# Kernel tuning notes

Hardware: AMD Instinct MI355X
Metric: run time of the kernel (lower is better)

## Reference

```python
import jax, jax.numpy as jnp
import numpy as np

UNITS = 1024


def setup_inputs() -> dict:
    key = jax.random.key(0)
    k1, k2, k3, k4, k5 = jax.random.split(key, 5)
    scale = 1.0 / np.sqrt(UNITS)
    return {
        "s_prev": jax.random.normal(k1, (32, UNITS), jnp.float32),
        "hidden_states": jax.random.normal(k2, (32, 4096, UNITS), jnp.float32),
        "W_w": jax.random.normal(k3, (UNITS, UNITS), jnp.float32) * scale,
        "W_b": jnp.zeros((UNITS,), jnp.float32),
        "U_w": jax.random.normal(k4, (UNITS, UNITS), jnp.float32) * scale,
        "U_b": jnp.zeros((UNITS,), jnp.float32),
        "V_w": jax.random.normal(k5, (UNITS, 1), jnp.float32) * scale,
        "V_b": jnp.zeros((1,), jnp.float32),
    }


def reference(s_prev, hidden_states, W_w, W_b, U_w, U_b, V_w, V_b):
    # s_prev: [B, U]; hidden_states: [B, S, U]
    w_s = s_prev @ W_w + W_b                      # [B, U]
    u_h = jnp.einsum("bsu,uv->bsv", hidden_states, U_w) + U_b  # [B, S, U]
    score = jnp.tanh(w_s[:, None, :] + u_h) @ V_w + V_b        # [B, S, 1]
    weights = jax.nn.softmax(score, axis=1)       # [B, S, 1]
    context = jnp.sum(weights * hidden_states, axis=1)         # [B, U]
    return context, weights
```

## Files before the change

kernel.cpp:

```cpp
#include <hip/hip_runtime.h>
#include <hip/hip_bf16.h>
#include <stdint.h>

typedef __attribute__((ext_vector_type(8))) short bf16x8;
typedef __attribute__((ext_vector_type(4))) float f32x4;
typedef __attribute__((ext_vector_type(2))) float f32x2;
typedef __attribute__((ext_vector_type(4))) short short4v;

#define UNITS 1024
#define BATCH 32
#define SEQ 4096
#define CHUNK 64
#define NCHUNK (SEQ / CHUNK)
#define PAD 8
#define LDK (UNITS + PAD)

static __device__ __forceinline__ float bf2f(unsigned short u) {
    union { unsigned int i; float f; } x; x.i = ((unsigned int)u) << 16; return x.f;
}
static __device__ __forceinline__ unsigned short f2bf(float f) {
    __hip_bfloat16 h = __float2bfloat16(f);
    return *reinterpret_cast<unsigned short*>(&h);
}
static __device__ __forceinline__ float fast_tanh(float x) {
    float e = __expf(2.0f * x);
    return 1.0f - 2.0f / (e + 1.0f);
}

__global__ void k_transpose_cast(const float* __restrict__ Uw,
                                 unsigned short* __restrict__ UwT) {
    __shared__ float tile[32][33];
    const int ti = blockIdx.x, tj = blockIdx.y;
    const int c = threadIdx.x;
    const int r0 = threadIdx.y;
#pragma unroll
    for (int rr = 0; rr < 4; ++rr) {
        int r = r0 + rr * 8;
        tile[r][c] = Uw[(size_t)(ti * 32 + r) * UNITS + tj * 32 + c];
    }
    __syncthreads();
#pragma unroll
    for (int rr = 0; rr < 4; ++rr) {
        int rv = r0 + rr * 8;
        UwT[(size_t)(tj * 32 + rv) * UNITS + ti * 32 + c] = f2bf(tile[c][rv]);
    }
}

__global__ void k_ws(const float* __restrict__ s_prev, const float* __restrict__ Ww,
                     const float* __restrict__ Wb, const float* __restrict__ Ub,
                     float* __restrict__ ws_vec) {
    const int b = blockIdx.y;
    const int v = blockIdx.x * 256 + threadIdx.x;
    const float* sp = s_prev + (size_t)b * UNITS;
    float acc = 0.f;
#pragma unroll 4
    for (int u = 0; u < UNITS; ++u)
        acc = fmaf(sp[u], Ww[(size_t)u * UNITS + v], acc);
    ws_vec[(size_t)b * UNITS + v] = acc + Wb[v] + Ub[v];
}

__launch_bounds__(512, 2)
__global__ void k_score_ctx(const float* __restrict__ hidden,
                            const unsigned short* __restrict__ UwT,
                            const float* __restrict__ ws_vec,
                            const float* __restrict__ Vw,
                            const float* __restrict__ Vb,
                            float* __restrict__ scores,
                            float* __restrict__ mstat,
                            float* __restrict__ lstat,
                            float* __restrict__ ctx_part) {
    __shared__ unsigned short h_lds[CHUNK * LDK];
    __shared__ float ws_lds[UNITS];
    __shared__ float v_lds[UNITS];
    __shared__ float scpart[8][CHUNK];
    __shared__ float sc_lds[CHUNK];
    __shared__ float esc[CHUNK];

    const int tid = threadIdx.x;
    const int bx  = blockIdx.x;
    const int b     = bx / NCHUNK;
    const int chunk = bx % NCHUNK;
    const int lane = tid & 63;
    const int w    = tid >> 6;
    const int l15  = lane & 15;
    const int l4   = lane >> 4;

    for (int i = tid; i < UNITS; i += 512) {
        ws_lds[i] = ws_vec[(size_t)b * UNITS + i];
        v_lds[i]  = Vw[i];
    }
    {
        const float* hbase = hidden + ((size_t)b * SEQ + (size_t)chunk * CHUNK) * UNITS;
        const int c4 = (tid & 255) * 4;
        const int rhalf = tid >> 8;
#pragma unroll 4
        for (int i = 0; i < 32; ++i) {
            int r = i * 2 + rhalf;
            f32x4 v = *reinterpret_cast<const f32x4*>(hbase + (size_t)r * UNITS + c4);
            short4v p;
            p.x = (short)f2bf(v.x); p.y = (short)f2bf(v.y);
            p.z = (short)f2bf(v.z); p.w = (short)f2bf(v.w);
            *reinterpret_cast<short4v*>(&h_lds[r * LDK + c4]) = p;
        }
    }
    __syncthreads();

    float spart[4][4];
#pragma unroll
    for (int fr = 0; fr < 4; ++fr)
#pragma unroll
        for (int j = 0; j < 4; ++j) spart[fr][j] = 0.f;

    for (int outer = 0; outer < 2; ++outer) {
        const int col0 = outer * 512 + w * 64;
        f32x4 acc[4][4];
#pragma unroll
        for (int fr = 0; fr < 4; ++fr)
#pragma unroll
            for (int fc = 0; fc < 4; ++fc) acc[fr][fc] = (f32x4)(0.f);

        for (int k0 = 0; k0 < UNITS; k0 += 32) {
            bf16x8 af[4], bf[4];
#pragma unroll
            for (int fr = 0; fr < 4; ++fr)
                af[fr] = *reinterpret_cast<const bf16x8*>(
                    &h_lds[(fr * 16 + l15) * LDK + k0 + l4 * 8]);
#pragma unroll
            for (int fc = 0; fc < 4; ++fc)
                bf[fc] = *reinterpret_cast<const bf16x8*>(
                    &UwT[(size_t)(col0 + fc * 16 + l15) * UNITS + k0 + l4 * 8]);
#pragma unroll
            for (int fr = 0; fr < 4; ++fr)
#pragma unroll
                for (int fc = 0; fc < 4; ++fc)
                    acc[fr][fc] = __builtin_amdgcn_mfma_f32_16x16x32_bf16(
                        af[fr], bf[fc], acc[fr][fc], 0, 0, 0);
        }
#pragma unroll
        for (int fc = 0; fc < 4; ++fc) {
            const int col = col0 + fc * 16 + l15;
            const float wsv = ws_lds[col];
            const float vv  = v_lds[col];
#pragma unroll
            for (int fr = 0; fr < 4; ++fr)
#pragma unroll
                for (int j = 0; j < 4; ++j) {
                    float t = fast_tanh(wsv + acc[fr][fc][j]);
                    spart[fr][j] = fmaf(t, vv, spart[fr][j]);
                }
        }
    }
#pragma unroll
    for (int fr = 0; fr < 4; ++fr)
#pragma unroll
        for (int j = 0; j < 4; ++j) {
            float v = spart[fr][j];
            v += __shfl_xor(v, 1);
            v += __shfl_xor(v, 2);
            v += __shfl_xor(v, 4);
            v += __shfl_xor(v, 8);
            spart[fr][j] = v;
        }
    if (l15 == 0) {
#pragma unroll
        for (int fr = 0; fr < 4; ++fr)
#pragma unroll
            for (int j = 0; j < 4; ++j)
                scpart[w][fr * 16 + l4 * 4 + j] = spart[fr][j];
    }
    __syncthreads();

    if (tid < CHUNK) {
        float sc = Vb[0];
#pragma unroll
        for (int ww = 0; ww < 8; ++ww) sc += scpart[ww][tid];
        scores[(size_t)b * SEQ + chunk * CHUNK + tid] = sc;
        sc_lds[tid] = sc;
    }
    __syncthreads();

    if (tid < 64) {
        float v = sc_lds[tid];
        float m = v;
#pragma unroll
        for (int mk = 1; mk < 64; mk <<= 1) m = fmaxf(m, __shfl_xor(m, mk));
        float e = __expf(v - m);
        esc[tid] = e;
        float l = e;
#pragma unroll
        for (int mk = 1; mk < 64; mk <<= 1) l += __shfl_xor(l, mk);
        if (tid == 0) {
            mstat[b * NCHUNK + chunk] = m;
            lstat[b * NCHUNK + chunk] = l;
        }
    }
    __syncthreads();

    {
        const int u0 = tid * 2;
        float a0 = 0.f, a1 = 0.f;
#pragma unroll 8
        for (int s = 0; s < CHUNK; ++s) {
            unsigned int p = *reinterpret_cast<const unsigned int*>(&h_lds[s * LDK + u0]);
            float e = esc[s];
            a0 = fmaf(e, bf2f((unsigned short)(p & 0xffffu)), a0);
            a1 = fmaf(e, bf2f((unsigned short)(p >> 16)), a1);
        }
        f32x2 o; o.x = a0; o.y = a1;
        *reinterpret_cast<f32x2*>(&ctx_part[((size_t)(b * NCHUNK + chunk)) * UNITS + u0]) = o;
    }
}

__global__ void k_weights(const float* __restrict__ scores, float* __restrict__ out_w) {
    const int b = blockIdx.x;
    const int tid = threadIdx.x;
    __shared__ float red[8];
    float sc[16];
#pragma unroll
    for (int i = 0; i < 16; ++i) sc[i] = scores[(size_t)b * SEQ + tid + i * 256];
    float m = sc[0];
#pragma unroll
    for (int i = 1; i < 16; ++i) m = fmaxf(m, sc[i]);
#pragma unroll
    for (int mk = 1; mk < 64; mk <<= 1) m = fmaxf(m, __shfl_xor(m, mk));
    if ((tid & 63) == 0) red[tid >> 6] = m;
    __syncthreads();
    m = fmaxf(fmaxf(red[0], red[1]), fmaxf(red[2], red[3]));
    __syncthreads();
    float l = 0.f;
#pragma unroll
    for (int i = 0; i < 16; ++i) { sc[i] = __expf(sc[i] - m); l += sc[i]; }
#pragma unroll
    for (int mk = 1; mk < 64; mk <<= 1) l += __shfl_xor(l, mk);
    if ((tid & 63) == 0) red[tid >> 6] = l;
    __syncthreads();
    l = red[0] + red[1] + red[2] + red[3];
    const float inv = 1.0f / l;
#pragma unroll
    for (int i = 0; i < 16; ++i)
        out_w[(size_t)b * SEQ + tid + i * 256] = sc[i] * inv;
}

__global__ void k_ctx_reduce(const float* __restrict__ mstat, const float* __restrict__ lstat,
                             const float* __restrict__ ctx_part, float* __restrict__ out_ctx) {
    const int b = blockIdx.x;
    const int tid = threadIdx.x;
    __shared__ float m_l[NCHUNK], l_l[NCHUNK], f_l[NCHUNK];
    if (tid < NCHUNK) { m_l[tid] = mstat[b * NCHUNK + tid]; l_l[tid] = lstat[b * NCHUNK + tid]; }
    __syncthreads();
    float M = -1e30f;
#pragma unroll 8
    for (int c = 0; c < NCHUNK; ++c) M = fmaxf(M, m_l[c]);
    __syncthreads();
    if (tid < NCHUNK) f_l[tid] = __expf(m_l[tid] - M);
    __syncthreads();
    float L = 0.f;
#pragma unroll 8
    for (int c = 0; c < NCHUNK; ++c) L += f_l[c] * l_l[c];
    const float inv = 1.0f / L;
    const int u = tid * 4;
    f32x4 acc = (f32x4)(0.f);
    for (int c = 0; c < NCHUNK; ++c) {
        float f = f_l[c];
        f32x4 v = *reinterpret_cast<const f32x4*>(
            &ctx_part[((size_t)(b * NCHUNK + c)) * UNITS + u]);
        acc.x = fmaf(f, v.x, acc.x);
        acc.y = fmaf(f, v.y, acc.y);
        acc.z = fmaf(f, v.z, acc.z);
        acc.w = fmaf(f, v.w, acc.w);
    }
    acc.x *= inv; acc.y *= inv; acc.z *= inv; acc.w *= inv;
    *reinterpret_cast<f32x4*>(&out_ctx[(size_t)b * UNITS + u]) = acc;
}

extern "C" void kernel_launch(void* const* d_in, const int* in_sizes, int n_in,
                              void* d_out, int out_size, void* d_ws, size_t ws_size,
                              hipStream_t stream) {
    const float* s_prev = (const float*)d_in[0];
    const float* hidden = (const float*)d_in[1];
    const float* Ww     = (const float*)d_in[2];
    const float* Wb     = (const float*)d_in[3];
    const float* Uw     = (const float*)d_in[4];
    const float* Ub     = (const float*)d_in[5];
    const float* Vw     = (const float*)d_in[6];
    const float* Vb     = (const float*)d_in[7];

    float* out_ctx = (float*)d_out;
    float* out_w   = (float*)d_out + BATCH * UNITS;

    char* wsb = (char*)d_ws;
    unsigned short* UwT = (unsigned short*)wsb;
    float* ws_vec = (float*)(wsb + (2u << 20));
    float* scores = (float*)(wsb + (2u << 20) + 131072);
    float* mstat  = (float*)(wsb + (2u << 20) + 131072 + 524288);
    float* lstat  = mstat + BATCH * NCHUNK;
    float* ctx_part = lstat + BATCH * NCHUNK;

    hipLaunchKernelGGL(k_transpose_cast, dim3(32, 32), dim3(32, 8), 0, stream, Uw, UwT);
    hipLaunchKernelGGL(k_ws, dim3(4, 32), dim3(256), 0, stream, s_prev, Ww, Wb, Ub, ws_vec);
    hipLaunchKernelGGL(k_score_ctx, dim3(BATCH * NCHUNK), dim3(512), 0, stream,
                       hidden, UwT, ws_vec, Vw, Vb, scores, mstat, lstat, ctx_part);
    hipLaunchKernelGGL(k_weights, dim3(BATCH), dim3(256), 0, stream, scores, out_w);
    hipLaunchKernelGGL(k_ctx_reduce, dim3(BATCH), dim3(256), 0, stream,
                       mstat, lstat, ctx_part, out_ctx);
}
```

Measured before the change: 1.305 ms.

## Persistent multi-chunk score kernel with pipelined hidden loads; split-K w_s GEMV

The score/context kernel now runs 256 persistent blocks, each handling 8 consecutive chunks. Hidden-state K-tiles are prefetched into registers two tiles ahead and converted into LDS while the MFMA work for the first column half runs, so global load latency overlaps compute. The w_s GEMV becomes a split-K kernel that keeps weight slices in registers and reuses them across the batch, followed by a reduction kernel. The trade-off is fewer blocks in flight (256 on a large GPU), more barriers per chunk, and higher register pressure from the prefetch buffers.

```diff
diff --git a/kernel.cpp b/kernel.cpp
--- a/kernel.cpp
+++ b/kernel.cpp
@@ -14,6 +14,9 @@
 #define NCHUNK (SEQ / CHUNK)
 #define PAD 8
 #define LDK (UNITS + PAD)
+#define BK 128
+#define NKT (UNITS / BK)
+#define TASKS 8
 
 static __device__ __forceinline__ float bf2f(unsigned short u) {
     union { unsigned int i; float f; } x; x.i = ((unsigned int)u) << 16; return x.f;
@@ -46,17 +49,41 @@
     }
 }
 
-__global__ void k_ws(const float* __restrict__ s_prev, const float* __restrict__ Ww,
-                     const float* __restrict__ Wb, const float* __restrict__ Ub,
-                     float* __restrict__ ws_vec) {
-    const int b = blockIdx.y;
-    const int v = blockIdx.x * 256 + threadIdx.x;
-    const float* sp = s_prev + (size_t)b * UNITS;
-    float acc = 0.f;
-#pragma unroll 4
-    for (int u = 0; u < UNITS; ++u)
-        acc = fmaf(sp[u], Ww[(size_t)u * UNITS + v], acc);
-    ws_vec[(size_t)b * UNITS + v] = acc + Wb[v] + Ub[v];
+__global__ void k_ws_part(const float* __restrict__ s_prev, const float* __restrict__ Ww,
+                          float* __restrict__ part) {
+    const int ks = blockIdx.x;
+    const int col0 = threadIdx.x * 4;
+    f32x4 wreg[32];
+#pragma unroll
+    for (int u = 0; u < 32; ++u)
+        wreg[u] = *reinterpret_cast<const f32x4*>(&Ww[(size_t)(ks * 32 + u) * UNITS + col0]);
+    for (int b = 0; b < BATCH; ++b) {
+        f32x4 acc = (f32x4)(0.f);
+#pragma unroll
+        for (int u = 0; u < 32; ++u) {
+            const float s = s_prev[(size_t)b * UNITS + ks * 32 + u];
+            acc.x = fmaf(s, wreg[u].x, acc.x);
+            acc.y = fmaf(s, wreg[u].y, acc.y);
+            acc.z = fmaf(s, wreg[u].z, acc.z);
+            acc.w = fmaf(s, wreg[u].w, acc.w);
+        }
+        *reinterpret_cast<f32x4*>(&part[((size_t)b * 32 + ks) * UNITS + col0]) = acc;
+    }
+}
+
+__global__ void k_ws_red(const float* __restrict__ part, const float* __restrict__ Wb,
+                         const float* __restrict__ Ub, float* __restrict__ ws_vec) {
+    const int b = blockIdx.x;
+    const int col0 = threadIdx.x * 4;
+    f32x4 acc = *reinterpret_cast<const f32x4*>(&Wb[col0]);
+    f32x4 ub  = *reinterpret_cast<const f32x4*>(&Ub[col0]);
+    acc.x += ub.x; acc.y += ub.y; acc.z += ub.z; acc.w += ub.w;
+#pragma unroll
+    for (int ks = 0; ks < 32; ++ks) {
+        f32x4 p = *reinterpret_cast<const f32x4*>(&part[((size_t)b * 32 + ks) * UNITS + col0]);
+        acc.x += p.x; acc.y += p.y; acc.z += p.z; acc.w += p.w;
+    }
+    *reinterpret_cast<f32x4*>(&ws_vec[(size_t)b * UNITS + col0]) = acc;
 }
 
 __launch_bounds__(512, 2)
@@ -73,141 +100,180 @@
     __shared__ float ws_lds[UNITS];
     __shared__ float v_lds[UNITS];
     __shared__ float scpart[8][CHUNK];
-    __shared__ float sc_lds[CHUNK];
     __shared__ float esc[CHUNK];
 
     const int tid = threadIdx.x;
-    const int bx  = blockIdx.x;
-    const int b     = bx / NCHUNK;
-    const int chunk = bx % NCHUNK;
+    const int blk = blockIdx.x;
+    const int b      = blk >> 3;
+    const int chunk0 = (blk & 7) * TASKS;
     const int lane = tid & 63;
     const int w    = tid >> 6;
     const int l15  = lane & 15;
     const int l4   = lane >> 4;
+    const int srow = tid >> 5;
+    const int sc0  = (tid & 31) * 4;
 
     for (int i = tid; i < UNITS; i += 512) {
         ws_lds[i] = ws_vec[(size_t)b * UNITS + i];
         v_lds[i]  = Vw[i];
     }
-    {
-        const float* hbase = hidden + ((size_t)b * SEQ + (size_t)chunk * CHUNK) * UNITS;
-        const int c4 = (tid & 255) * 4;
-        const int rhalf = tid >> 8;
-#pragma unroll 4
-        for (int i = 0; i < 32; ++i) {
-            int r = i * 2 + rhalf;
-            f32x4 v = *reinterpret_cast<const f32x4*>(hbase + (size_t)r * UNITS + c4);
-            short4v p;
-            p.x = (short)f2bf(v.x); p.y = (short)f2bf(v.y);
-            p.z = (short)f2bf(v.z); p.w = (short)f2bf(v.w);
-            *reinterpret_cast<short4v*>(&h_lds[r * LDK + c4]) = p;
-        }
-    }
-    __syncthreads();
-
-    float spart[4][4];
-#pragma unroll
-    for (int fr = 0; fr < 4; ++fr)
-#pragma unroll
-        for (int j = 0; j < 4; ++j) spart[fr][j] = 0.f;
-
-    for (int outer = 0; outer < 2; ++outer) {
-        const int col0 = outer * 512 + w * 64;
-        f32x4 acc[4][4];
-#pragma unroll
-        for (int fr = 0; fr < 4; ++fr)
-#pragma unroll
-            for (int fc = 0; fc < 4; ++fc) acc[fr][fc] = (f32x4)(0.f);
-
-        for (int k0 = 0; k0 < UNITS; k0 += 32) {
-            bf16x8 af[4], bf[4];
+    const float vb0 = Vb[0];
+
+    auto issue = [&](const float* hb, int kt, f32x4* P) {
+#pragma unroll
+        for (int j = 0; j < 4; ++j)
+            P[j] = *reinterpret_cast<const f32x4*>(
+                hb + (size_t)(srow + j * 16) * UNITS + kt * BK + sc0);
+    };
+    auto swrite = [&](int kt, f32x4* P) {
+#pragma unroll
+        for (int j = 0; j < 4; ++j) {
+            short4v s;
+            s.x = (short)f2bf(P[j].x); s.y = (short)f2bf(P[j].y);
+            s.z = (short)f2bf(P[j].z); s.w = (short)f2bf(P[j].w);
+            *reinterpret_cast<short4v*>(&h_lds[(srow + j * 16) * LDK + kt * BK + sc0]) = s;
+        }
+    };
+    auto gemm_tile = [&](int kt, f32x4 (&acc)[4][4], int colbase) {
+#pragma unroll
+        for (int ks = 0; ks < 4; ++ks) {
+            const int k0 = kt * BK + ks * 32;
+            bf16x8 af[4], bfr[4];
 #pragma unroll
             for (int fr = 0; fr < 4; ++fr)
                 af[fr] = *reinterpret_cast<const bf16x8*>(
                     &h_lds[(fr * 16 + l15) * LDK + k0 + l4 * 8]);
 #pragma unroll
             for (int fc = 0; fc < 4; ++fc)
-                bf[fc] = *reinterpret_cast<const bf16x8*>(
-                    &UwT[(size_t)(col0 + fc * 16 + l15) * UNITS + k0 + l4 * 8]);
+                bfr[fc] = *reinterpret_cast<const bf16x8*>(
+                    &UwT[(size_t)(colbase + fc * 16 + l15) * UNITS + k0 + l4 * 8]);
 #pragma unroll
             for (int fr = 0; fr < 4; ++fr)
 #pragma unroll
                 for (int fc = 0; fc < 4; ++fc)
                     acc[fr][fc] = __builtin_amdgcn_mfma_f32_16x16x32_bf16(
-                        af[fr], bf[fc], acc[fr][fc], 0, 0, 0);
-        }
+                        af[fr], bfr[fc], acc[fr][fc], 0, 0, 0);
+        }
+    };
+    auto epi = [&](f32x4 (&acc)[4][4], int colbase, float (&spart)[4][4]) {
 #pragma unroll
         for (int fc = 0; fc < 4; ++fc) {
-            const int col = col0 + fc * 16 + l15;
+            const int col = colbase + fc * 16 + l15;
             const float wsv = ws_lds[col];
             const float vv  = v_lds[col];
 #pragma unroll
             for (int fr = 0; fr < 4; ++fr)
 #pragma unroll
-                for (int j = 0; j < 4; ++j) {
-                    float t = fast_tanh(wsv + acc[fr][fc][j]);
-                    spart[fr][j] = fmaf(t, vv, spart[fr][j]);
-                }
-        }
-    }
-#pragma unroll
-    for (int fr = 0; fr < 4; ++fr)
-#pragma unroll
-        for (int j = 0; j < 4; ++j) {
-            float v = spart[fr][j];
-            v += __shfl_xor(v, 1);
-            v += __shfl_xor(v, 2);
-            v += __shfl_xor(v, 4);
-            v += __shfl_xor(v, 8);
-            spart[fr][j] = v;
-        }
-    if (l15 == 0) {
+                for (int j = 0; j < 4; ++j)
+                    spart[fr][j] = fmaf(fast_tanh(wsv + acc[fr][fc][j]), vv, spart[fr][j]);
+        }
+    };
+
+    f32x4 PA[4], PB[4];
+    {
+        const float* hb0 = hidden + ((size_t)b * SEQ + (size_t)chunk0 * CHUNK) * UNITS;
+        issue(hb0, 0, PA);
+        issue(hb0, 1, PB);
+    }
+
+    for (int t = 0; t < TASKS; ++t) {
+        const int chunk = chunk0 + t;
+        const float* hb  = hidden + ((size_t)b * SEQ + (size_t)chunk * CHUNK) * UNITS;
+        const int tn = (t < TASKS - 1) ? t + 1 : t;
+        const float* hbn = hidden + ((size_t)b * SEQ + (size_t)(chunk0 + tn) * CHUNK) * UNITS;
+
+        float spart[4][4];
 #pragma unroll
         for (int fr = 0; fr < 4; ++fr)
 #pragma unroll
-            for (int j = 0; j < 4; ++j)
-                scpart[w][fr * 16 + l4 * 4 + j] = spart[fr][j];
-    }
-    __syncthreads();
-
-    if (tid < CHUNK) {
-        float sc = Vb[0];
-#pragma unroll
-        for (int ww = 0; ww < 8; ++ww) sc += scpart[ww][tid];
-        scores[(size_t)b * SEQ + chunk * CHUNK + tid] = sc;
-        sc_lds[tid] = sc;
-    }
-    __syncthreads();
-
-    if (tid < 64) {
-        float v = sc_lds[tid];
-        float m = v;
-#pragma unroll
-        for (int mk = 1; mk < 64; mk <<= 1) m = fmaxf(m, __shfl_xor(m, mk));
-        float e = __expf(v - m);
-        esc[tid] = e;
-        float l = e;
-#pragma unroll
-        for (int mk = 1; mk < 64; mk <<= 1) l += __shfl_xor(l, mk);
-        if (tid == 0) {
-            mstat[b * NCHUNK + chunk] = m;
-            lstat[b * NCHUNK + chunk] = l;
-        }
-    }
-    __syncthreads();
-
-    {
-        const int u0 = tid * 2;
-        float a0 = 0.f, a1 = 0.f;
+            for (int j = 0; j < 4; ++j) spart[fr][j] = 0.f;
+
+        f32x4 acc[4][4];
+#pragma unroll
+        for (int fr = 0; fr < 4; ++fr)
+#pragma unroll
+            for (int fc = 0; fc < 4; ++fc) acc[fr][fc] = (f32x4)(0.f);
+
+#pragma unroll
+        for (int kp = 0; kp < 4; ++kp) {
+            const int kt0 = kp * 2, kt1 = kp * 2 + 1;
+            swrite(kt0, PA);
+            if (kt0 + 2 < NKT) issue(hb, kt0 + 2, PA);
+            else               issue(hbn, kt0 + 2 - NKT, PA);
+            __syncthreads();
+            gemm_tile(kt0, acc, w * 64);
+            swrite(kt1, PB);
+            if (kt1 + 2 < NKT) issue(hb, kt1 + 2, PB);
+            else               issue(hbn, kt1 + 2 - NKT, PB);
+            __syncthreads();
+            gemm_tile(kt1, acc, w * 64);
+        }
+        epi(acc, w * 64, spart);
+
+#pragma unroll
+        for (int fr = 0; fr < 4; ++fr)
+#pragma unroll
+            for (int fc = 0; fc < 4; ++fc) acc[fr][fc] = (f32x4)(0.f);
+#pragma unroll 2
+        for (int kt = 0; kt < NKT; ++kt)
+            gemm_tile(kt, acc, 512 + w * 64);
+        epi(acc, 512 + w * 64, spart);
+
+#pragma unroll
+        for (int fr = 0; fr < 4; ++fr)
+#pragma unroll
+            for (int j = 0; j < 4; ++j) {
+                float v = spart[fr][j];
+                v += __shfl_xor(v, 1);
+                v += __shfl_xor(v, 2);
+                v += __shfl_xor(v, 4);
+                v += __shfl_xor(v, 8);
+                spart[fr][j] = v;
+            }
+        if (l15 == 0) {
+#pragma unroll
+            for (int fr = 0; fr < 4; ++fr)
+#pragma unroll
+                for (int j = 0; j < 4; ++j)
+                    scpart[w][fr * 16 + l4 * 4 + j] = spart[fr][j];
+        }
+        __syncthreads();
+
+        if (tid < CHUNK) {
+            float sc = vb0;
+#pragma unroll
+            for (int ww = 0; ww < 8; ++ww) sc += scpart[ww][tid];
+            scores[(size_t)b * SEQ + chunk * CHUNK + tid] = sc;
+            float m = sc;
+#pragma unroll
+            for (int mk = 1; mk < 64; mk <<= 1) m = fmaxf(m, __shfl_xor(m, mk));
+            float e = __expf(sc - m);
+            esc[tid] = e;
+            float l = e;
+#pragma unroll
+            for (int mk = 1; mk < 64; mk <<= 1) l += __shfl_xor(l, mk);
+            if (tid == 0) {
+                mstat[b * NCHUNK + chunk] = m;
+                lstat[b * NCHUNK + chunk] = l;
+            }
+        }
+        __syncthreads();
+
+        {
+            const int u0 = tid * 2;
+            float a0 = 0.f, a1 = 0.f;
 #pragma unroll 8
-        for (int s = 0; s < CHUNK; ++s) {
-            unsigned int p = *reinterpret_cast<const unsigned int*>(&h_lds[s * LDK + u0]);
-            float e = esc[s];
-            a0 = fmaf(e, bf2f((unsigned short)(p & 0xffffu)), a0);
-            a1 = fmaf(e, bf2f((unsigned short)(p >> 16)), a1);
-        }
-        f32x2 o; o.x = a0; o.y = a1;
-        *reinterpret_cast<f32x2*>(&ctx_part[((size_t)(b * NCHUNK + chunk)) * UNITS + u0]) = o;
+            for (int s = 0; s < CHUNK; ++s) {
+                unsigned int p = *reinterpret_cast<const unsigned int*>(&h_lds[s * LDK + u0]);
+                float e = esc[s];
+                a0 = fmaf(e, bf2f((unsigned short)(p & 0xffffu)), a0);
+                a1 = fmaf(e, bf2f((unsigned short)(p >> 16)), a1);
+            }
+            f32x2 o; o.x = a0; o.y = a1;
+            *reinterpret_cast<f32x2*>(
+                &ctx_part[((size_t)(b * NCHUNK + chunk)) * UNITS + u0]) = o;
+        }
+        __syncthreads();
     }
 }
 
@@ -260,6 +326,7 @@
     const float inv = 1.0f / L;
     const int u = tid * 4;
     f32x4 acc = (f32x4)(0.f);
+#pragma unroll 4
     for (int c = 0; c < NCHUNK; ++c) {
         float f = f_l[c];
         f32x4 v = *reinterpret_cast<const f32x4*>(
@@ -295,10 +362,12 @@
     float* mstat  = (float*)(wsb + (2u << 20) + 131072 + 524288);
     float* lstat  = mstat + BATCH * NCHUNK;
     float* ctx_part = lstat + BATCH * NCHUNK;
+    float* ws_part  = ctx_part;
 
     hipLaunchKernelGGL(k_transpose_cast, dim3(32, 32), dim3(32, 8), 0, stream, Uw, UwT);
-    hipLaunchKernelGGL(k_ws, dim3(4, 32), dim3(256), 0, stream, s_prev, Ww, Wb, Ub, ws_vec);
-    hipLaunchKernelGGL(k_score_ctx, dim3(BATCH * NCHUNK), dim3(512), 0, stream,
+    hipLaunchKernelGGL(k_ws_part, dim3(32), dim3(256), 0, stream, s_prev, Ww, ws_part);
+    hipLaunchKernelGGL(k_ws_red, dim3(BATCH), dim3(256), 0, stream, ws_part, Wb, Ub, ws_vec);
+    hipLaunchKernelGGL(k_score_ctx, dim3(256), dim3(512), 0, stream,
                        hidden, UwT, ws_vec, Vw, Vb, scores, mstat, lstat, ctx_part);
     hipLaunchKernelGGL(k_weights, dim3(BATCH), dim3(256), 0, stream, scores, out_w);
     hipLaunchKernelGGL(k_ctx_reduce, dim3(BATCH), dim3(256), 0, stream,
```

Result: slower. 1.475 ms (+13.1%).
